# Kernel tuning notes

Hardware: AMD Instinct MI355X
Metric: run time of the kernel (lower is better)

## Reference

```python
import jax, jax.numpy as jnp
import numpy as np

# ---- constant kernels (kornia canny defaults) ----

def _gauss_kernel1d(ksize=5, sigma=1.0):
    x = np.arange(ksize, dtype=np.float32) - (ksize - 1) / 2.0
    g = np.exp(-(x ** 2) / (2.0 * sigma ** 2))
    return (g / g.sum()).astype(np.float32)

_GK = _gauss_kernel1d()
_SOBEL_X = np.array([[-1, 0, 1], [-2, 0, 2], [-1, 0, 1]], np.float32) / 8.0  # normalized=True
_SOBEL_Y = _SOBEL_X.T.copy()

# 8 directional NMS kernels: +1 at center, -1 at neighbor d*45 degrees (kornia order)
_NMS = np.zeros((8, 1, 3, 3), np.float32)
_OFFS = [(0, 1), (1, 1), (1, 0), (1, -1), (0, -1), (-1, -1), (-1, 0), (-1, 1)]
for _i, (_dy, _dx) in enumerate(_OFFS):
    _NMS[_i, 0, 1, 1] = 1.0
    _NMS[_i, 0, 1 + _dy, 1 + _dx] = -1.0


def _conv(x, k):
    return jax.lax.conv_general_dilated(
        x, k, (1, 1), 'VALID', dimension_numbers=('NCHW', 'OIHW', 'NCHW'))


def _canny_dilate(x):
    # x: [B,3,H,W] BGR in [0,1]
    x = x[:, ::-1]  # bgr -> rgb
    gray = 0.299 * x[:, 0:1] + 0.587 * x[:, 1:2] + 0.114 * x[:, 2:3]  # [B,1,H,W]

    # gaussian blur 5x5, sigma=1, reflect padding (separable)
    p = jnp.pad(gray, ((0, 0), (0, 0), (2, 2), (2, 2)), mode='reflect')
    kh = jnp.asarray(_GK).reshape(1, 1, 1, 5)
    kv = jnp.asarray(_GK).reshape(1, 1, 5, 1)
    blurred = _conv(_conv(p, kh), kv)

    # sobel gradients, replicate padding
    sp = jnp.pad(blurred, ((0, 0), (0, 0), (1, 1), (1, 1)), mode='edge')
    sob = jnp.asarray(np.stack([_SOBEL_X, _SOBEL_Y])[:, None])  # (2,1,3,3)
    g = _conv(sp, sob)
    gx, gy = g[:, 0:1], g[:, 1:2]

    mag = jnp.sqrt(gx * gx + gy * gy + 1e-6)  # [B,1,H,W]
    ang45 = jnp.round(jnp.arctan2(gy, gx) * (180.0 / np.pi) / 45.0)  # multiples of 45 deg
    pos_idx = jnp.mod(ang45, 8).astype(jnp.int32)
    neg_idx = jnp.mod(ang45 + 4, 8).astype(jnp.int32)

    # direction-dependent non-maximum suppression
    nms = _conv(jnp.pad(mag, ((0, 0), (0, 0), (1, 1), (1, 1))), jnp.asarray(_NMS))  # [B,8,H,W]
    pos = jnp.take_along_axis(nms, pos_idx, axis=1)
    neg = jnp.take_along_axis(nms, neg_idx, axis=1)
    is_max = jnp.minimum(pos, neg) > 0.0
    mag = mag * is_max

    # morphological dilation, 5x5 ones kernel, geodesic border (pad with -max_val)
    MAX_VAL = 1e4
    padded = jnp.pad(mag, ((0, 0), (0, 0), (2, 2), (2, 2)), constant_values=-MAX_VAL)
    out = jax.lax.reduce_window(padded, -jnp.inf, jax.lax.max,
                                (1, 1, 5, 5), (1, 1, 1, 1), 'VALID')
    return out


def setup_inputs() -> dict:
    key = jax.random.key(0)
    x = jax.random.uniform(key, (32, 3, 512, 512), dtype=jnp.float32)
    return {'x': x}


def reference(x):
    return _canny_dilate(x)
```

## Files before the change

kernel.cpp:

```cpp
#include <hip/hip_runtime.h>
#include <math.h>

#define IMW 512
#define SEG 23
#define NSEG 23
#define NSTRIP 10
#define OUTW 52
#define TRIPS (SEG + 12)

__device__ __forceinline__ int reflect512(int i) {
    int a = i < 0 ? -i : i;
    int b = 1022 - a;
    return a < b ? a : b;
}
__device__ __forceinline__ float bperm(int a4, float v) {
    return __int_as_float(__builtin_amdgcn_ds_bpermute(a4, __float_as_int(v)));
}

template<bool EDGE>
__device__ __forceinline__ void pipe_run(
    const float* __restrict__ base0, const float* __restrict__ base1,
    const float* __restrict__ base2, float* __restrict__ outp,
    int Y0, int xr, bool inimg, bool stlane, int l4, int aL4, int aR4)
{
    const float K0 = 0.054488684549643f, K1 = 0.244201342003233f, K2 = 0.402619946931554f;

    float hb[5], hx[5], hy[5], mg[5], cm[5];
    int   ax[5];
    #pragma unroll
    for (int i = 0; i < 5; ++i) { hb[i]=0.f; hx[i]=0.f; hy[i]=0.f; mg[i]=0.f; cm[i]=0.f; ax[i]=0; }

    int r0i = Y0 - 6;
    if (EDGE) r0i = reflect512(r0i);
    float p0 = (base0 + (size_t)r0i * IMW)[xr];
    float p1 = (base1 + (size_t)r0i * IMW)[xr];
    float p2 = (base2 + (size_t)r0i * IMW)[xr];

    #pragma unroll 5
    for (int t = 0; t < TRIPS; ++t) {
        const int v = Y0 - 6 + t;

        float gray = 0.299f * p2 + 0.587f * p1 + 0.114f * p0;
        int rn = v + 1;
        if (EDGE) rn = reflect512(rn);
        const float* r0 = base0 + (size_t)rn * IMW;
        const float* r1 = base1 + (size_t)rn * IMW;
        const float* r2 = base2 + (size_t)rn * IMW;
        p0 = r0[xr]; p1 = r1[xr]; p2 = r2[xr];

        float gl1 = bperm(l4 - 4, gray), gl2 = bperm(l4 - 8, gray);
        float gr1 = bperm(l4 + 4, gray), gr2 = bperm(l4 + 8, gray);
        hb[t % 5] = K0 * (gl2 + gr2) + K1 * (gl1 + gr1) + K2 * gray;

        float blur = K0 * (hb[(t + 1) % 5] + hb[t % 5])
                   + K1 * (hb[(t + 2) % 5] + hb[(t + 4) % 5])
                   + K2 * hb[(t + 3) % 5];

        float bl = bperm(aL4, blur), br = bperm(aR4, blur);
        hx[t % 5] = br - bl;
        hy[t % 5] = bl + 2.f * blur + br;

        float hxa, hxc, hya, hyc;
        if (EDGE) {
            const int g = v - 3;
            hxa = (g == 0)   ? hx[(t + 4) % 5] : hx[(t + 3) % 5];
            hya = (g == 0)   ? hy[(t + 4) % 5] : hy[(t + 3) % 5];
            hxc = (g == 511) ? hx[(t + 4) % 5] : hx[t % 5];
            hyc = (g == 511) ? hy[(t + 4) % 5] : hy[t % 5];
        } else {
            hxa = hx[(t + 3) % 5]; hya = hy[(t + 3) % 5];
            hxc = hx[t % 5];       hyc = hy[t % 5];
        }
        float gxv = (hxa + 2.f * hx[(t + 4) % 5] + hxc) * 0.125f;
        float gyv = (hyc - hya) * 0.125f;
        float mag = sqrtf(gxv * gxv + gyv * gyv + 1e-6f);
        float axm = fabsf(gxv), aym = fabsf(gyv);
        int axis;
        if (aym <= 0.41421356237309515f * axm)      axis = 0;
        else if (aym >= 2.4142135623730951f * axm)  axis = 2;
        else axis = ((gxv >= 0.f) == (gyv >= 0.f)) ? 1 : 3;
        mg[t % 5] = inimg ? mag : 0.f;
        ax[t % 5] = axis;

        const int m = v - 4;
        float magc = mg[(t + 4) % 5];
        float magp, magm;
        if (EDGE) {
            magp = (m >= 511) ? 0.f : mg[t % 5];
            magm = (m <= 0)   ? 0.f : mg[(t + 3) % 5];
        } else {
            magp = mg[t % 5];
            magm = mg[(t + 3) % 5];
        }
        float gcp = bperm(l4 + 4, magc), gcm = bperm(l4 - 4, magc);
        float gpp = bperm(l4 + 4, magp), gpm = bperm(l4 - 4, magp);
        float gmm = bperm(l4 - 4, magm), gmp = bperm(l4 + 4, magm);
        int d = ax[(t + 4) % 5];
        float mp = (d == 0) ? gcp : (d == 1) ? gpp : (d == 2) ? magp : gpm;
        float mn = (d == 0) ? gcm : (d == 1) ? gmm : (d == 2) ? magm : gmp;
        bool keep = fminf(magc - mp, magc - mn) > 0.f;
        if (EDGE) keep = keep && (m >= 0) && (m <= 511);
        float msk = keep ? magc : 0.f;

        float s1 = fmaxf(bperm(l4 - 4, msk), bperm(l4 + 4, msk));
        float s2 = fmaxf(bperm(l4 - 8, msk), bperm(l4 + 8, msk));
        cm[t % 5] = fmaxf(fmaxf(s1, s2), msk);

        if (t >= 12) {
            const int y = v - 6;
            float c0 = cm[(t + 1) % 5], c1 = cm[(t + 2) % 5];
            float c2 = cm[(t + 3) % 5];
            float c3 = cm[(t + 4) % 5], c4 = cm[t % 5];
            if (EDGE) {
                if (y < 2)   { c0 = 0.f; if (y < 1)   c1 = 0.f; }
                if (y > 509) { c4 = 0.f; if (y > 510) c3 = 0.f; }
            }
            float val = fmaxf(fmaxf(fmaxf(c0, c1), fmaxf(c2, c3)), c4);
            if ((!EDGE || y < 512) && stlane)
                outp[(size_t)y * IMW] = val;
        }
    }
}

__global__ __launch_bounds__(256)
void canny_pipe(const float* __restrict__ x, float* __restrict__ out) {
    const int lane  = threadIdx.x & 63;
    const int unit  = blockIdx.x * 4 + (threadIdx.x >> 6);
    const int img   = unit / (NSTRIP * NSEG);
    const int rem   = unit - img * (NSTRIP * NSEG);
    const int strip = rem / NSEG;
    const int seg   = rem - strip * NSEG;
    const int Y0 = seg * SEG;
    const int x0 = strip * OUTW - 6;
    const int xv = x0 + lane;
    const int xr = reflect512(xv);
    const bool inimg  = (xv >= 0) && (xv < IMW);
    const bool stlane = (lane >= 6) && (lane < 58) && (xv < IMW);
    const int l4  = lane << 2;
    const int aL4 = (min(max(xv - 1, 0), 511) - x0) << 2;
    const int aR4 = (min(max(xv + 1, 0), 511) - x0) << 2;

    const float* base = x + (size_t)img * 3 * IMW * IMW;
    const float* b0 = base;
    const float* b1 = base + (size_t)IMW * IMW;
    const float* b2 = base + (size_t)2 * IMW * IMW;
    float* outp = out + (size_t)img * IMW * IMW + xv;

    if (seg >= 1 && seg <= 20)
        pipe_run<false>(b0, b1, b2, outp, Y0, xr, inimg, stlane, l4, aL4, aR4);
    else
        pipe_run<true >(b0, b1, b2, outp, Y0, xr, inimg, stlane, l4, aL4, aR4);
}

extern "C" void kernel_launch(void* const* d_in, const int* in_sizes, int n_in,
                              void* d_out, int out_size, void* d_ws, size_t ws_size,
                              hipStream_t stream) {
    const float* x = (const float*)d_in[0];
    float* out = (float*)d_out;
    const int units = 32 * NSTRIP * NSEG;
    dim3 grid(units / 4);
    canny_pipe<<<grid, 256, 0, stream>>>(x, out);
}
```

Baseline: 181.9 us.

## Process two columns per lane with float2 loads, widening strips to reduce halo overhead

Each lane now handles an even/odd column pair, loading float2 per channel and computing both pipelines, so a 64-lane wave covers 128 columns with 116 outputs instead of 52. This cuts the redundant horizontal halo work and the number of strips, halves bpermute count per output pixel, and separates x-edge and y-edge specializations into four template variants. Last strip and segment are shifted inward so they overlap rather than run past the image edge. Register pressure roughly doubles, which may lower occupancy.

```diff
diff --git a/kernel.cpp b/kernel.cpp
--- a/kernel.cpp
+++ b/kernel.cpp
@@ -4,9 +4,9 @@
 #define IMW 512
 #define SEG 23
 #define NSEG 23
-#define NSTRIP 10
-#define OUTW 52
-#define TRIPS (SEG + 12)
+#define NSTRIP 5
+#define OUTW 116
+#define ITERS 7
 
 __device__ __forceinline__ int reflect512(int i) {
     int a = i < 0 ? -i : i;
@@ -17,107 +17,141 @@
     return __int_as_float(__builtin_amdgcn_ds_bpermute(a4, __float_as_int(v)));
 }
 
-template<bool EDGE>
+template<bool XE, bool YE>
 __device__ __forceinline__ void pipe_run(
-    const float* __restrict__ base0, const float* __restrict__ base1,
-    const float* __restrict__ base2, float* __restrict__ outp,
-    int Y0, int xr, bool inimg, bool stlane, int l4, int aL4, int aR4)
+    const float* __restrict__ c0p, const float* __restrict__ c1p,
+    const float* __restrict__ c2p, float* __restrict__ outp,
+    int Y0, int cb, bool inimgE, bool inimgO, bool stl,
+    int lm4, int lp4, int srcE4, int srcO4, bool clampL, bool clampR)
 {
     const float K0 = 0.054488684549643f, K1 = 0.244201342003233f, K2 = 0.402619946931554f;
 
-    float hb[5], hx[5], hy[5], mg[5], cm[5];
-    int   ax[5];
+    float hbE[5],hbO[5],hxE[5],hxO[5],hyE[5],hyO[5],mgE[5],mgO[5],cmE[5],cmO[5];
+    int axE[5], axO[5];
     #pragma unroll
-    for (int i = 0; i < 5; ++i) { hb[i]=0.f; hx[i]=0.f; hy[i]=0.f; mg[i]=0.f; cm[i]=0.f; ax[i]=0; }
-
-    int r0i = Y0 - 6;
-    if (EDGE) r0i = reflect512(r0i);
-    float p0 = (base0 + (size_t)r0i * IMW)[xr];
-    float p1 = (base1 + (size_t)r0i * IMW)[xr];
-    float p2 = (base2 + (size_t)r0i * IMW)[xr];
-
-    #pragma unroll 5
-    for (int t = 0; t < TRIPS; ++t) {
-        const int v = Y0 - 6 + t;
-
-        float gray = 0.299f * p2 + 0.587f * p1 + 0.114f * p0;
-        int rn = v + 1;
-        if (EDGE) rn = reflect512(rn);
-        const float* r0 = base0 + (size_t)rn * IMW;
-        const float* r1 = base1 + (size_t)rn * IMW;
-        const float* r2 = base2 + (size_t)rn * IMW;
-        p0 = r0[xr]; p1 = r1[xr]; p2 = r2[xr];
-
-        float gl1 = bperm(l4 - 4, gray), gl2 = bperm(l4 - 8, gray);
-        float gr1 = bperm(l4 + 4, gray), gr2 = bperm(l4 + 8, gray);
-        hb[t % 5] = K0 * (gl2 + gr2) + K1 * (gl1 + gr1) + K2 * gray;
-
-        float blur = K0 * (hb[(t + 1) % 5] + hb[t % 5])
-                   + K1 * (hb[(t + 2) % 5] + hb[(t + 4) % 5])
-                   + K2 * hb[(t + 3) % 5];
-
-        float bl = bperm(aL4, blur), br = bperm(aR4, blur);
-        hx[t % 5] = br - bl;
-        hy[t % 5] = bl + 2.f * blur + br;
-
-        float hxa, hxc, hya, hyc;
-        if (EDGE) {
+    for (int i = 0; i < 5; ++i) {
+        hbE[i]=0.f;hbO[i]=0.f;hxE[i]=0.f;hxO[i]=0.f;hyE[i]=0.f;hyO[i]=0.f;
+        mgE[i]=0.f;mgO[i]=0.f;cmE[i]=0.f;cmO[i]=0.f;axE[i]=0;axO[i]=0;
+    }
+
+    int r0 = Y0 - 6;
+    if (YE) r0 = reflect512(r0);
+    float2 p0 = *(const float2*)(c0p + (size_t)r0 * IMW + cb);
+    float2 p1 = *(const float2*)(c1p + (size_t)r0 * IMW + cb);
+    float2 p2 = *(const float2*)(c2p + (size_t)r0 * IMW + cb);
+
+    for (int it = 0; it < ITERS; ++it) {
+        #pragma unroll
+        for (int j = 0; j < 5; ++j) {
+            const int t = it * 5 + j;
+            const int v = Y0 - 6 + t;
+
+            float gE = 0.299f * p2.x + 0.587f * p1.x + 0.114f * p0.x;
+            float gO = 0.299f * p2.y + 0.587f * p1.y + 0.114f * p0.y;
+            int rn = v + 1;
+            rn = YE ? reflect512(rn) : min(rn, 511);
+            const float* q0 = c0p + (size_t)rn * IMW;
+            const float* q1 = c1p + (size_t)rn * IMW;
+            const float* q2 = c2p + (size_t)rn * IMW;
+            p0 = *(const float2*)(q0 + cb);
+            p1 = *(const float2*)(q1 + cb);
+            p2 = *(const float2*)(q2 + cb);
+
+            if (XE) { gE = bperm(srcE4, gE); gO = bperm(srcO4, gO); }
+
+            float eL = bperm(lm4, gE), eR = bperm(lp4, gE);
+            float oL = bperm(lm4, gO), oR = bperm(lp4, gO);
+            hbE[j] = K0 * (eL + eR) + K1 * (oL + gO) + K2 * gE;
+            hbO[j] = K0 * (oL + oR) + K1 * (gE + eR) + K2 * gO;
+
+            float bE = K0 * (hbE[(j+1)%5] + hbE[j]) + K1 * (hbE[(j+2)%5] + hbE[(j+4)%5]) + K2 * hbE[(j+3)%5];
+            float bO = K0 * (hbO[(j+1)%5] + hbO[j]) + K1 * (hbO[(j+2)%5] + hbO[(j+4)%5]) + K2 * hbO[(j+3)%5];
+
+            float oLb = bperm(lm4, bO);
+            float eRb = bperm(lp4, bE);
+            float nblE = XE ? (clampL ? bE : oLb) : oLb;
+            float nbrO = XE ? (clampR ? bO : eRb) : eRb;
+            hxE[j] = bO - nblE;
+            hyE[j] = nblE + 2.f * bE + bO;
+            hxO[j] = nbrO - bE;
+            hyO[j] = bE + 2.f * bO + nbrO;
+
             const int g = v - 3;
-            hxa = (g == 0)   ? hx[(t + 4) % 5] : hx[(t + 3) % 5];
-            hya = (g == 0)   ? hy[(t + 4) % 5] : hy[(t + 3) % 5];
-            hxc = (g == 511) ? hx[(t + 4) % 5] : hx[t % 5];
-            hyc = (g == 511) ? hy[(t + 4) % 5] : hy[t % 5];
-        } else {
-            hxa = hx[(t + 3) % 5]; hya = hy[(t + 3) % 5];
-            hxc = hx[t % 5];       hyc = hy[t % 5];
-        }
-        float gxv = (hxa + 2.f * hx[(t + 4) % 5] + hxc) * 0.125f;
-        float gyv = (hyc - hya) * 0.125f;
-        float mag = sqrtf(gxv * gxv + gyv * gyv + 1e-6f);
-        float axm = fabsf(gxv), aym = fabsf(gyv);
-        int axis;
-        if (aym <= 0.41421356237309515f * axm)      axis = 0;
-        else if (aym >= 2.4142135623730951f * axm)  axis = 2;
-        else axis = ((gxv >= 0.f) == (gyv >= 0.f)) ? 1 : 3;
-        mg[t % 5] = inimg ? mag : 0.f;
-        ax[t % 5] = axis;
-
-        const int m = v - 4;
-        float magc = mg[(t + 4) % 5];
-        float magp, magm;
-        if (EDGE) {
-            magp = (m >= 511) ? 0.f : mg[t % 5];
-            magm = (m <= 0)   ? 0.f : mg[(t + 3) % 5];
-        } else {
-            magp = mg[t % 5];
-            magm = mg[(t + 3) % 5];
-        }
-        float gcp = bperm(l4 + 4, magc), gcm = bperm(l4 - 4, magc);
-        float gpp = bperm(l4 + 4, magp), gpm = bperm(l4 - 4, magp);
-        float gmm = bperm(l4 - 4, magm), gmp = bperm(l4 + 4, magm);
-        int d = ax[(t + 4) % 5];
-        float mp = (d == 0) ? gcp : (d == 1) ? gpp : (d == 2) ? magp : gpm;
-        float mn = (d == 0) ? gcm : (d == 1) ? gmm : (d == 2) ? magm : gmp;
-        bool keep = fminf(magc - mp, magc - mn) > 0.f;
-        if (EDGE) keep = keep && (m >= 0) && (m <= 511);
-        float msk = keep ? magc : 0.f;
-
-        float s1 = fmaxf(bperm(l4 - 4, msk), bperm(l4 + 4, msk));
-        float s2 = fmaxf(bperm(l4 - 8, msk), bperm(l4 + 8, msk));
-        cm[t % 5] = fmaxf(fmaxf(s1, s2), msk);
-
-        if (t >= 12) {
-            const int y = v - 6;
-            float c0 = cm[(t + 1) % 5], c1 = cm[(t + 2) % 5];
-            float c2 = cm[(t + 3) % 5];
-            float c3 = cm[(t + 4) % 5], c4 = cm[t % 5];
-            if (EDGE) {
-                if (y < 2)   { c0 = 0.f; if (y < 1)   c1 = 0.f; }
-                if (y > 509) { c4 = 0.f; if (y > 510) c3 = 0.f; }
-            }
-            float val = fmaxf(fmaxf(fmaxf(c0, c1), fmaxf(c2, c3)), c4);
-            if ((!EDGE || y < 512) && stlane)
-                outp[(size_t)y * IMW] = val;
+            float hxaE, hxcE, hyaE, hycE, hxaO, hxcO, hyaO, hycO;
+            if (YE) {
+                hxaE = (g == 0)   ? hxE[(j+4)%5] : hxE[(j+3)%5];
+                hyaE = (g == 0)   ? hyE[(j+4)%5] : hyE[(j+3)%5];
+                hxcE = (g == 511) ? hxE[(j+4)%5] : hxE[j];
+                hycE = (g == 511) ? hyE[(j+4)%5] : hyE[j];
+                hxaO = (g == 0)   ? hxO[(j+4)%5] : hxO[(j+3)%5];
+                hyaO = (g == 0)   ? hyO[(j+4)%5] : hyO[(j+3)%5];
+                hxcO = (g == 511) ? hxO[(j+4)%5] : hxO[j];
+                hycO = (g == 511) ? hyO[(j+4)%5] : hyO[j];
+            } else {
+                hxaE = hxE[(j+3)%5]; hyaE = hyE[(j+3)%5]; hxcE = hxE[j]; hycE = hyE[j];
+                hxaO = hxO[(j+3)%5]; hyaO = hyO[(j+3)%5]; hxcO = hxO[j]; hycO = hyO[j];
+            }
+            float gxE = (hxaE + 2.f * hxE[(j+4)%5] + hxcE) * 0.125f;
+            float gyE = (hycE - hyaE) * 0.125f;
+            float gxO = (hxaO + 2.f * hxO[(j+4)%5] + hxcO) * 0.125f;
+            float gyO = (hycO - hyaO) * 0.125f;
+            float magE = sqrtf(gxE * gxE + gyE * gyE + 1e-6f);
+            float magO = sqrtf(gxO * gxO + gyO * gyO + 1e-6f);
+            {
+                float axm = fabsf(gxE), aym = fabsf(gyE);
+                axE[j] = (aym <= 0.41421356237309515f * axm) ? 0
+                       : (aym >= 2.4142135623730951f  * axm) ? 2
+                       : (((gxE >= 0.f) == (gyE >= 0.f)) ? 1 : 3);
+            }
+            {
+                float axm = fabsf(gxO), aym = fabsf(gyO);
+                axO[j] = (aym <= 0.41421356237309515f * axm) ? 0
+                       : (aym >= 2.4142135623730951f  * axm) ? 2
+                       : (((gxO >= 0.f) == (gyO >= 0.f)) ? 1 : 3);
+            }
+            mgE[j] = inimgE ? magE : 0.f;
+            mgO[j] = inimgO ? magO : 0.f;
+
+            const int m = v - 4;
+            float magcE = mgE[(j+4)%5], magcO = mgO[(j+4)%5];
+            float magpE = mgE[j],       magpO = mgO[j];
+            float magmE = mgE[(j+3)%5], magmO = mgO[(j+3)%5];
+            if (YE) {
+                if (m >= 511) { magpE = 0.f; magpO = 0.f; }
+                if (m <= 0)   { magmE = 0.f; magmO = 0.f; }
+            }
+            float oLc = bperm(lm4, magcO), eRc = bperm(lp4, magcE);
+            float oLp = bperm(lm4, magpO), eRp = bperm(lp4, magpE);
+            float oLm = bperm(lm4, magmO), eRm = bperm(lp4, magmE);
+            int dE = axE[(j+4)%5], dO = axO[(j+4)%5];
+            float mpE = (dE == 0) ? magcO : (dE == 1) ? magpO : (dE == 2) ? magpE : oLp;
+            float mnE = (dE == 0) ? oLc   : (dE == 1) ? oLm   : (dE == 2) ? magmE : magmO;
+            float mpO = (dO == 0) ? eRc   : (dO == 1) ? eRp   : (dO == 2) ? magpO : magpE;
+            float mnO = (dO == 0) ? magcE : (dO == 1) ? magmE : (dO == 2) ? magmO : eRm;
+            float mskE = (fminf(magcE - mpE, magcE - mnE) > 0.f) ? magcE : 0.f;
+            float mskO = (fminf(magcO - mpO, magcO - mnO) > 0.f) ? magcO : 0.f;
+
+            float eLk = bperm(lm4, mskE), eRk = bperm(lp4, mskE);
+            float oLk = bperm(lm4, mskO), oRk = bperm(lp4, mskO);
+            float c4 = fmaxf(fmaxf(oLk, mskE), fmaxf(mskO, eRk));
+            cmE[j] = fmaxf(c4, eLk);
+            cmO[j] = fmaxf(c4, oRk);
+
+            if (t >= 12) {
+                const int y = v - 6;
+                float e0 = cmE[(j+1)%5], e1 = cmE[(j+2)%5], e2 = cmE[(j+3)%5];
+                float e3 = cmE[(j+4)%5], e4 = cmE[j];
+                float o0 = cmO[(j+1)%5], o1 = cmO[(j+2)%5], o2 = cmO[(j+3)%5];
+                float o3 = cmO[(j+4)%5], o4 = cmO[j];
+                if (YE) {
+                    if (y < 2)   { e0 = 0.f; o0 = 0.f; if (y < 1)   { e1 = 0.f; o1 = 0.f; } }
+                    if (y > 509) { e4 = 0.f; o4 = 0.f; if (y > 510) { e3 = 0.f; o3 = 0.f; } }
+                }
+                float2 val;
+                val.x = fmaxf(fmaxf(fmaxf(e0, e1), fmaxf(e2, e3)), e4);
+                val.y = fmaxf(fmaxf(fmaxf(o0, o1), fmaxf(o2, o3)), o4);
+                if (stl) *(float2*)(outp + (size_t)y * IMW) = val;
+            }
         }
     }
 }
@@ -130,26 +164,35 @@
     const int rem   = unit - img * (NSTRIP * NSEG);
     const int strip = rem / NSEG;
     const int seg   = rem - strip * NSEG;
-    const int Y0 = seg * SEG;
-    const int x0 = strip * OUTW - 6;
-    const int xv = x0 + lane;
-    const int xr = reflect512(xv);
-    const bool inimg  = (xv >= 0) && (xv < IMW);
-    const bool stlane = (lane >= 6) && (lane < 58) && (xv < IMW);
-    const int l4  = lane << 2;
-    const int aL4 = (min(max(xv - 1, 0), 511) - x0) << 2;
-    const int aR4 = (min(max(xv + 1, 0), 511) - x0) << 2;
+
+    int Y0 = seg * SEG;       if (seg == NSEG - 1)    Y0 = 512 - SEG;
+    int Xs = strip * OUTW;    if (strip == NSTRIP - 1) Xs = 512 - OUTW;
+    const int X0 = Xs - 6;
+    const int ce = X0 + 2 * lane, co = ce + 1;
+    const int cb = min(max(ce, 0), 510);
+    const bool inimgE = (unsigned)ce < 512u;
+    const bool inimgO = (unsigned)co < 512u;
+    const bool stl = (lane >= 3) && (lane <= 60);
+    const int lm4 = (lane - 1) << 2, lp4 = (lane + 1) << 2;
+    const int srcE4 = ((reflect512(min(max(ce, -2), 512)) - X0) >> 1) << 2;
+    const int srcO4 = ((reflect512(min(max(co, -1), 513)) - X0 - 1) >> 1) << 2;
+    const bool clampL = (ce == 0), clampR = (co == 511);
 
     const float* base = x + (size_t)img * 3 * IMW * IMW;
-    const float* b0 = base;
-    const float* b1 = base + (size_t)IMW * IMW;
-    const float* b2 = base + (size_t)2 * IMW * IMW;
-    float* outp = out + (size_t)img * IMW * IMW + xv;
-
-    if (seg >= 1 && seg <= 20)
-        pipe_run<false>(b0, b1, b2, outp, Y0, xr, inimg, stlane, l4, aL4, aR4);
-    else
-        pipe_run<true >(b0, b1, b2, outp, Y0, xr, inimg, stlane, l4, aL4, aR4);
+    const float* c0p = base;
+    const float* c1p = base + (size_t)IMW * IMW;
+    const float* c2p = base + (size_t)2 * IMW * IMW;
+    float* outp = out + (size_t)img * IMW * IMW + ce;
+
+    const bool xe = (strip == 0) || (strip == NSTRIP - 1);
+    const bool ye = (seg == 0) || (seg == NSEG - 1);
+    if (xe) {
+        if (ye) pipe_run<true , true >(c0p,c1p,c2p,outp,Y0,cb,inimgE,inimgO,stl,lm4,lp4,srcE4,srcO4,clampL,clampR);
+        else    pipe_run<true , false>(c0p,c1p,c2p,outp,Y0,cb,inimgE,inimgO,stl,lm4,lp4,srcE4,srcO4,clampL,clampR);
+    } else {
+        if (ye) pipe_run<false, true >(c0p,c1p,c2p,outp,Y0,cb,inimgE,inimgO,stl,lm4,lp4,srcE4,srcO4,clampL,clampR);
+        else    pipe_run<false, false>(c0p,c1p,c2p,outp,Y0,cb,inimgE,inimgO,stl,lm4,lp4,srcE4,srcO4,clampL,clampR);
+    }
 }
 
 extern "C" void kernel_launch(void* const* d_in, const int* in_sizes, int n_in,
```

After: 175.7 us. 1.04x faster.
